# Performance work log

Hardware: AMD Instinct MI355X
Metric: run time of the kernel (lower is better)

## Reference

```python
import jax, jax.numpy as jnp
import numpy as np

B = 4096        # args.batch_size
M = 2           # n_views (and m in approximate_hsic_zy)
N = B * M       # total rows after torch.cat of views
D = 128         # projector feature dim
GAMMA = 3.0     # args.gamma
SIGMA = 1.0     # Gaussian kernel bandwidth used by compute_gaussian_kernel


def setup_inputs() -> dict:
    key = jax.random.key(0)
    x = jax.random.normal(key, (N, D), dtype=jnp.float32)
    # module applies l2_norm (F.normalize dim=1) before hsic_objective
    feat = x / jnp.maximum(jnp.linalg.norm(x, axis=1, keepdims=True), 1e-12)
    return {"feat": feat}


def _gaussian_kernel(x, y):
    # pairwise squared distances via the GEMM trick, then Gaussian kernel
    sq = (jnp.sum(x * x, axis=1)[:, None]
          + jnp.sum(y * y, axis=1)[None, :]
          - 2.0 * (x @ y.T))
    sq = jnp.maximum(sq, 0.0)
    return jnp.exp(-sq / (2.0 * SIGMA * SIGMA))


def _approximate_hsic_zy(K):
    # labels = cat([arange(B)]*M); labels-equality matrix; exclude diagonal.
    lab = jnp.tile(jnp.arange(B), M)                      # [N]
    eq = (lab[:, None] == lab[None, :]).astype(K.dtype)   # [N,N]
    offdiag = 1.0 - jnp.eye(N, dtype=K.dtype)
    # positives / negatives sums over off-diagonal entries (same math as the
    # boolean-mask view/reshape in torch, expressed as masked reductions)
    pos_sum = jnp.sum(K * eq * offdiag)
    neg_sum = jnp.sum(K * (1.0 - eq) * offdiag)
    term_1 = pos_sum / (B * M * (M - 1))
    term_2 = neg_sum / (B ** 2 * M ** 2)
    term_3 = 1.0 / (M - 1)
    scale = B / (B - 1.0)  # get_label_weights(batch_size) stand-in
    return scale * (term_1 - term_2 - term_3)


def _hsic_regular(K):
    # HSIC(z,z) with doubly-centered kernel: mean(Kc * Kc) since Kx == Ky
    row_m = jnp.mean(K, axis=0, keepdims=True)
    col_m = jnp.mean(K, axis=1, keepdims=True)
    tot_m = jnp.mean(K)
    Kc = K - row_m - col_m + tot_m
    return jnp.mean(Kc * Kc)


def reference(feat):
    K = _gaussian_kernel(feat, feat)          # [N,N] pairwise Gaussian kernel
    hsic_zy = _approximate_hsic_zy(K)
    hsic_zz = _hsic_regular(K)
    return -hsic_zy + GAMMA * jnp.sqrt(hsic_zz)
```

## Files before the change

### kernel.cpp

```cpp
#include <hip/hip_runtime.h>
#include <hip/hip_bf16.h>


using bf16   = __bf16;
using bf16x8 = __attribute__((ext_vector_type(8))) __bf16;
using f32x4  = __attribute__((ext_vector_type(4))) float;

#define N_ROWS 8192
#define LOG2E  1.4426950408889634f

__global__ __launch_bounds__(256) void prep_kernel(
    const float* __restrict__ feat, unsigned short* __restrict__ xb,
    float* __restrict__ h) {
  const int w = threadIdx.x >> 6, lane = threadIdx.x & 63;
  const int row = blockIdx.x * 4 + w;
  const float2 x2 = ((const float2*)feat)[row * 64 + lane];
  float ss = x2.x * x2.x + x2.y * x2.y;
#pragma unroll
  for (int m = 1; m < 64; m <<= 1) ss += __shfl_xor(ss, m);
  if (lane == 0) h[row] = 0.5f * ss;
  const unsigned int ux = __float_as_uint(x2.x);
  const unsigned int uy = __float_as_uint(x2.y);
  ushort2 o;
  o.x = (unsigned short)((ux + 0x7FFFu + ((ux >> 16) & 1u)) >> 16);
  o.y = (unsigned short)((uy + 0x7FFFu + ((uy >> 16) & 1u)) >> 16);
  ((ushort2*)xb)[row * 64 + lane] = o;
}

__global__ __launch_bounds__(256, 2) void gram_kernel(
    const bf16* __restrict__ xb, const float* __restrict__ h,
    float* __restrict__ rpart, float* __restrict__ bscal) {
  const int bjc = blockIdx.x, bi = blockIdx.y;
  const int tid = threadIdx.x, lane = tid & 63, w = tid >> 6;
  const int wr = w >> 1, wc = w & 1;
  const int l15 = lane & 15, l4 = lane >> 4;
  const int arow0 = bi * 128 + wr * 64;

  __shared__ float rbuf[128];
  __shared__ float sS[4], sD[4], sP[4];
  if (tid < 128) rbuf[tid] = 0.f;
  __syncthreads();

  bf16x8 a[4][4];
  float ha[4][4];
#pragma unroll
  for (int ks = 0; ks < 4; ++ks)
#pragma unroll
    for (int f = 0; f < 4; ++f)
      a[ks][f] =
          *(const bf16x8*)(xb + (arow0 + f * 16 + l15) * 128 + ks * 32 + l4 * 8);
#pragma unroll
  for (int fr = 0; fr < 4; ++fr)
#pragma unroll
    for (int e = 0; e < 4; ++e)
      ha[fr][e] = h[arow0 + fr * 16 + l4 * 4 + e];

  float rsum[4][4] = {};
  float s2 = 0.f, pdiag = 0.f, ppos = 0.f;

  for (int t = 0; t < 8; ++t) {
    const int bj = bjc * 8 + t;
    const int brow0 = bj * 128 + wc * 64;

    f32x4 acc[4][4] = {};
#pragma unroll
    for (int ks = 0; ks < 4; ++ks) {
      bf16x8 b[4];
#pragma unroll
      for (int f = 0; f < 4; ++f)
        b[f] = *(const bf16x8*)(xb + (brow0 + f * 16 + l15) * 128 + ks * 32 +
                                l4 * 8);
#pragma unroll
      for (int fr = 0; fr < 4; ++fr)
#pragma unroll
        for (int fc = 0; fc < 4; ++fc)
          acc[fr][fc] = __builtin_amdgcn_mfma_f32_16x16x32_bf16(
              a[ks][fr], b[fc], acc[fr][fc], 0, 0, 0);
    }

    float hb[4];
#pragma unroll
    for (int fc = 0; fc < 4; ++fc) hb[fc] = h[brow0 + fc * 16 + l15];

    const int dt = bj - bi;
    const bool isdiag = (dt == 0);
    const bool ispos = (dt == 32) || (dt == -32);

#pragma unroll
    for (int fr = 0; fr < 4; ++fr) {
#pragma unroll
      for (int fc = 0; fc < 4; ++fc) {
        const int cc = wc * 64 + fc * 16 + l15;
#pragma unroll
        for (int e = 0; e < 4; ++e) {
          const float dot = acc[fr][fc][e];
          const float me = fminf(dot - ha[fr][e] - hb[fc], 0.f);
          const float K = exp2f(me * LOG2E);
          s2 = fmaf(K, K, s2);
          rsum[fr][e] += K;
          if (isdiag | ispos) {
            const int rr = wr * 64 + fr * 16 + l4 * 4 + e;
            const float hit = (rr == cc) ? K : 0.f;
            if (isdiag) pdiag += hit;
            else ppos += hit;
          }
        }
      }
    }
  }

#pragma unroll
  for (int fr = 0; fr < 4; ++fr) {
#pragma unroll
    for (int e = 0; e < 4; ++e) {
      float r = rsum[fr][e];
      r += __shfl_xor(r, 1);
      r += __shfl_xor(r, 2);
      r += __shfl_xor(r, 4);
      r += __shfl_xor(r, 8);
      if (l15 == 0) atomicAdd(&rbuf[wr * 64 + fr * 16 + l4 * 4 + e], r);
    }
  }

#pragma unroll
  for (int m = 1; m < 64; m <<= 1) {
    s2 += __shfl_xor(s2, m);
    pdiag += __shfl_xor(pdiag, m);
    ppos += __shfl_xor(ppos, m);
  }
  if (lane == 0) { sS[w] = s2; sD[w] = pdiag; sP[w] = ppos; }
  __syncthreads();

  const int slot = bi * 8 + bjc;
  if (tid < 128) rpart[slot * 128 + tid] = rbuf[tid];
  if (tid == 0) {
    bscal[slot * 3 + 0] = sS[0] + sS[1] + sS[2] + sS[3];
    bscal[slot * 3 + 1] = sD[0] + sD[1] + sD[2] + sD[3];
    bscal[slot * 3 + 2] = sP[0] + sP[1] + sP[2] + sP[3];
  }
}

__global__ __launch_bounds__(256) void final_kernel(
    const float* __restrict__ rpart, const float* __restrict__ bscal,
    float* __restrict__ out) {
  const int tid = threadIdx.x, lane = tid & 63, w = tid >> 6;
  double t = 0.0, v2 = 0.0, s2 = 0.0, dg = 0.0, ps = 0.0;
  for (int i = tid; i < N_ROWS; i += 256) {
    const int rb = i >> 7, r = i & 127;
    float s = 0.f;
#pragma unroll
    for (int c = 0; c < 8; ++c) s += rpart[(rb * 8 + c) * 128 + r];
    const double x = (double)s;
    t += x;
    v2 += x * x;
  }
  for (int i = tid; i < 512; i += 256) {
    s2 += (double)bscal[i * 3 + 0];
    dg += (double)bscal[i * 3 + 1];
    ps += (double)bscal[i * 3 + 2];
  }
#pragma unroll
  for (int m = 1; m < 64; m <<= 1) {
    t += __shfl_xor(t, m);
    v2 += __shfl_xor(v2, m);
    s2 += __shfl_xor(s2, m);
    dg += __shfl_xor(dg, m);
    ps += __shfl_xor(ps, m);
  }
  __shared__ double sh[5][4];
  if (lane == 0) {
    sh[0][w] = t; sh[1][w] = v2; sh[2][w] = s2; sh[3][w] = dg; sh[4][w] = ps;
  }
  __syncthreads();
  if (tid == 0) {
    const double T  = sh[0][0] + sh[0][1] + sh[0][2] + sh[0][3];
    const double V2 = sh[1][0] + sh[1][1] + sh[1][2] + sh[1][3];
    const double S2 = sh[2][0] + sh[2][1] + sh[2][2] + sh[2][3];
    const double DG = sh[3][0] + sh[3][1] + sh[3][2] + sh[3][3];
    const double PS = sh[4][0] + sh[4][1] + sh[4][2] + sh[4][3];
    const double Nd = 8192.0, Bd = 4096.0;
    const double hzz = (S2 - (2.0 / Nd) * V2 + (T * T) / (Nd * Nd)) / (Nd * Nd);
    const double neg = (T - DG) - PS;
    const double t1 = PS / 8192.0;
    const double t2 = neg / 67108864.0;
    const double hzy = (Bd / (Bd - 1.0)) * (t1 - t2 - 1.0);
    out[0] = (float)(-hzy + 3.0 * sqrt(fmax(hzz, 0.0)));
  }
}

extern "C" void kernel_launch(void* const* d_in, const int* in_sizes, int n_in,
                              void* d_out, int out_size, void* d_ws,
                              size_t ws_size, hipStream_t stream) {
  (void)in_sizes; (void)n_in; (void)out_size; (void)ws_size;
  const float* feat = (const float*)d_in[0];
  char* ws = (char*)d_ws;
  unsigned short* xb = (unsigned short*)ws;
  float* h     = (float*)(ws + 2097152);
  float* rpart = (float*)(ws + 2097152 + 32768);
  float* bscal = (float*)(ws + 2097152 + 32768 + 262144);
  float* out = (float*)d_out;

  prep_kernel<<<2048, 256, 0, stream>>>(feat, xb, h);
  gram_kernel<<<dim3(8, 64), 256, 0, stream>>>((const bf16*)xb, h, rpart, bscal);
  final_kernel<<<1, 256, 0, stream>>>(rpart, bscal, out);
}
```

Measured before the change: 131.8 us.

## Stage A tile in swizzled LDS, fold log2e into inputs, raise occupancy

The A-row tile now lives in XOR-swizzled LDS instead of 64 registers per thread. Launch bounds go up to 4 blocks per CU, and the grid doubles to 16x64 with 4 column tiles per block. The log2e factor is folded into the bf16 features (via sqrt(log2e)) and into the norm term, and the MFMA accumulators start at -ha-hb, so the epilogue is just min and exp2. The intent is to cut register pressure and per-element ALU work so more waves can hide load and exp latency. In exchange it adds LDS reads per MFMA step, more partial slots for the final reduction, and extra bf16 rounding from the scaled inputs.

```diff
diff --git a/kernel.cpp b/kernel.cpp
--- a/kernel.cpp
+++ b/kernel.cpp
@@ -7,62 +7,80 @@
 using f32x4  = __attribute__((ext_vector_type(4))) float;
 
 #define N_ROWS 8192
-#define LOG2E  1.4426950408889634f
+#define SQRT_LOG2E 1.2011224087864498f
+#define LOG2E      1.4426950408889634f
 
 __global__ __launch_bounds__(256) void prep_kernel(
     const float* __restrict__ feat, unsigned short* __restrict__ xb,
-    float* __restrict__ h) {
+    float* __restrict__ hp) {
   const int w = threadIdx.x >> 6, lane = threadIdx.x & 63;
   const int row = blockIdx.x * 4 + w;
   const float2 x2 = ((const float2*)feat)[row * 64 + lane];
   float ss = x2.x * x2.x + x2.y * x2.y;
 #pragma unroll
   for (int m = 1; m < 64; m <<= 1) ss += __shfl_xor(ss, m);
-  if (lane == 0) h[row] = 0.5f * ss;
-  const unsigned int ux = __float_as_uint(x2.x);
-  const unsigned int uy = __float_as_uint(x2.y);
+  if (lane == 0) hp[row] = 0.5f * LOG2E * ss;
+  const unsigned int ux = __float_as_uint(x2.x * SQRT_LOG2E);
+  const unsigned int uy = __float_as_uint(x2.y * SQRT_LOG2E);
   ushort2 o;
   o.x = (unsigned short)((ux + 0x7FFFu + ((ux >> 16) & 1u)) >> 16);
   o.y = (unsigned short)((uy + 0x7FFFu + ((uy >> 16) & 1u)) >> 16);
   ((ushort2*)xb)[row * 64 + lane] = o;
 }
 
-__global__ __launch_bounds__(256, 2) void gram_kernel(
-    const bf16* __restrict__ xb, const float* __restrict__ h,
+__global__ __launch_bounds__(256, 4) void gram_kernel(
+    const bf16* __restrict__ xb, const float* __restrict__ hp,
     float* __restrict__ rpart, float* __restrict__ bscal) {
   const int bjc = blockIdx.x, bi = blockIdx.y;
   const int tid = threadIdx.x, lane = tid & 63, w = tid >> 6;
   const int wr = w >> 1, wc = w & 1;
   const int l15 = lane & 15, l4 = lane >> 4;
-  const int arow0 = bi * 128 + wr * 64;
-
+
+  __shared__ char  lds_a[32768];
+  __shared__ float lds_ha[128];
   __shared__ float rbuf[128];
   __shared__ float sS[4], sD[4], sP[4];
-  if (tid < 128) rbuf[tid] = 0.f;
+
+  {
+    const int rowbase = bi * 128;
+#pragma unroll
+    for (int i = 0; i < 8; ++i) {
+      const int c = tid + i * 256;
+      const int row = c >> 4;
+      const int byteoff = (c & 15) << 4;
+      const bf16x8 vv =
+          *(const bf16x8*)(xb + (rowbase + row) * 128 + (byteoff >> 1));
+      const int sw = ((row << 8) | byteoff) ^ ((row & 7) << 4);
+      *(bf16x8*)(lds_a + sw) = vv;
+    }
+    if (tid < 128) {
+      lds_ha[tid] = hp[rowbase + tid];
+      rbuf[tid] = 0.f;
+    }
+  }
   __syncthreads();
 
-  bf16x8 a[4][4];
-  float ha[4][4];
-#pragma unroll
-  for (int ks = 0; ks < 4; ++ks)
-#pragma unroll
-    for (int f = 0; f < 4; ++f)
-      a[ks][f] =
-          *(const bf16x8*)(xb + (arow0 + f * 16 + l15) * 128 + ks * 32 + l4 * 8);
-#pragma unroll
-  for (int fr = 0; fr < 4; ++fr)
-#pragma unroll
-    for (int e = 0; e < 4; ++e)
-      ha[fr][e] = h[arow0 + fr * 16 + l4 * 4 + e];
-
   float rsum[4][4] = {};
-  float s2 = 0.f, pdiag = 0.f, ppos = 0.f;
-
-  for (int t = 0; t < 8; ++t) {
-    const int bj = bjc * 8 + t;
+  float s2a = 0.f, s2b = 0.f, pdiag = 0.f, ppos = 0.f;
+
+  for (int t = 0; t < 4; ++t) {
+    const int bj = bjc * 4 + t;
     const int brow0 = bj * 128 + wc * 64;
 
-    f32x4 acc[4][4] = {};
+    float hb[4];
+#pragma unroll
+    for (int fc = 0; fc < 4; ++fc) hb[fc] = hp[brow0 + fc * 16 + l15];
+
+    f32x4 acc[4][4];
+#pragma unroll
+    for (int fr = 0; fr < 4; ++fr) {
+      const f32x4 hav = *(const f32x4*)(&lds_ha[wr * 64 + fr * 16 + l4 * 4]);
+#pragma unroll
+      for (int fc = 0; fc < 4; ++fc)
+#pragma unroll
+        for (int e = 0; e < 4; ++e) acc[fr][fc][e] = -hav[e] - hb[fc];
+    }
+
 #pragma unroll
     for (int ks = 0; ks < 4; ++ks) {
       bf16x8 b[4];
@@ -71,38 +89,36 @@
         b[f] = *(const bf16x8*)(xb + (brow0 + f * 16 + l15) * 128 + ks * 32 +
                                 l4 * 8);
 #pragma unroll
-      for (int fr = 0; fr < 4; ++fr)
+      for (int fr = 0; fr < 4; ++fr) {
+        const int arow = wr * 64 + fr * 16 + l15;
+        const int byte = (arow << 8) + ks * 64 + (l4 << 4);
+        const bf16x8 a = *(const bf16x8*)(lds_a + (byte ^ ((arow & 7) << 4)));
 #pragma unroll
         for (int fc = 0; fc < 4; ++fc)
           acc[fr][fc] = __builtin_amdgcn_mfma_f32_16x16x32_bf16(
-              a[ks][fr], b[fc], acc[fr][fc], 0, 0, 0);
-    }
-
-    float hb[4];
-#pragma unroll
-    for (int fc = 0; fc < 4; ++fc) hb[fc] = h[brow0 + fc * 16 + l15];
+              a, b[fc], acc[fr][fc], 0, 0, 0);
+      }
+    }
 
     const int dt = bj - bi;
-    const bool isdiag = (dt == 0);
-    const bool ispos = (dt == 32) || (dt == -32);
+    const bool isd = (dt == 0);
+    const bool isp = (dt == 32) | (dt == -32);
 
 #pragma unroll
     for (int fr = 0; fr < 4; ++fr) {
 #pragma unroll
       for (int fc = 0; fc < 4; ++fc) {
-        const int cc = wc * 64 + fc * 16 + l15;
 #pragma unroll
         for (int e = 0; e < 4; ++e) {
-          const float dot = acc[fr][fc][e];
-          const float me = fminf(dot - ha[fr][e] - hb[fc], 0.f);
-          const float K = exp2f(me * LOG2E);
-          s2 = fmaf(K, K, s2);
+          const float me = fminf(acc[fr][fc][e], 0.f);
+          const float K = exp2f(me);
+          if (fc & 1) s2b = fmaf(K, K, s2b); else s2a = fmaf(K, K, s2a);
           rsum[fr][e] += K;
-          if (isdiag | ispos) {
+          if (isd | isp) {
             const int rr = wr * 64 + fr * 16 + l4 * 4 + e;
+            const int cc = wc * 64 + fc * 16 + l15;
             const float hit = (rr == cc) ? K : 0.f;
-            if (isdiag) pdiag += hit;
-            else ppos += hit;
+            if (isd) pdiag += hit; else ppos += hit;
           }
         }
       }
@@ -121,7 +137,7 @@
       if (l15 == 0) atomicAdd(&rbuf[wr * 64 + fr * 16 + l4 * 4 + e], r);
     }
   }
-
+  float s2 = s2a + s2b;
 #pragma unroll
   for (int m = 1; m < 64; m <<= 1) {
     s2 += __shfl_xor(s2, m);
@@ -131,7 +147,7 @@
   if (lane == 0) { sS[w] = s2; sD[w] = pdiag; sP[w] = ppos; }
   __syncthreads();
 
-  const int slot = bi * 8 + bjc;
+  const int slot = bi * 16 + bjc;
   if (tid < 128) rpart[slot * 128 + tid] = rbuf[tid];
   if (tid == 0) {
     bscal[slot * 3 + 0] = sS[0] + sS[1] + sS[2] + sS[3];
@@ -149,12 +165,12 @@
     const int rb = i >> 7, r = i & 127;
     float s = 0.f;
 #pragma unroll
-    for (int c = 0; c < 8; ++c) s += rpart[(rb * 8 + c) * 128 + r];
+    for (int c = 0; c < 16; ++c) s += rpart[(rb * 16 + c) * 128 + r];
     const double x = (double)s;
     t += x;
     v2 += x * x;
   }
-  for (int i = tid; i < 512; i += 256) {
+  for (int i = tid; i < 1024; i += 256) {
     s2 += (double)bscal[i * 3 + 0];
     dg += (double)bscal[i * 3 + 1];
     ps += (double)bscal[i * 3 + 2];
@@ -195,12 +211,13 @@
   const float* feat = (const float*)d_in[0];
   char* ws = (char*)d_ws;
   unsigned short* xb = (unsigned short*)ws;
-  float* h     = (float*)(ws + 2097152);
+  float* hp    = (float*)(ws + 2097152);
   float* rpart = (float*)(ws + 2097152 + 32768);
-  float* bscal = (float*)(ws + 2097152 + 32768 + 262144);
+  float* bscal = (float*)(ws + 2097152 + 32768 + 524288);
   float* out = (float*)d_out;
 
-  prep_kernel<<<2048, 256, 0, stream>>>(feat, xb, h);
-  gram_kernel<<<dim3(8, 64), 256, 0, stream>>>((const bf16*)xb, h, rpart, bscal);
+  prep_kernel<<<2048, 256, 0, stream>>>(feat, xb, hp);
+  gram_kernel<<<dim3(16, 64), 256, 0, stream>>>((const bf16*)xb, hp, rpart,
+                                                bscal);
   final_kernel<<<1, 256, 0, stream>>>(rpart, bscal, out);
 }
```

New measurement: 183.2 us. 1.39x slower.
